# Kernel tuning notes

Hardware: AMD Instinct MI355X
Metric: run time of the kernel (lower is better)

## Reference

```python
import jax, jax.numpy as jnp
import numpy as np

B, V, VD = 4, 256, 3
H_DIM, N_HEADS = 512, 8
HEAD_DIM = H_DIM // N_HEADS
LN_EPS = 1e-5


def _ln(x, g, b):
    m = jnp.mean(x, axis=-1, keepdims=True)
    v = jnp.var(x, axis=-1, keepdims=True)
    return (x - m) * jax.lax.rsqrt(v + LN_EPS) * g + b


def setup_inputs() -> dict:
    key = jax.random.key(0)
    ks = jax.random.split(key, 20)
    s = lambda fan_in: 1.0 / np.sqrt(fan_in)
    return {
        "vertices": jax.random.normal(ks[0], (B, V, VD), jnp.float32),
        # vertex_proj: Linear(3 -> 512)
        "wp": jax.random.uniform(ks[1], (H_DIM, VD), jnp.float32, -s(VD), s(VD)),
        "bp": jax.random.uniform(ks[2], (H_DIM,), jnp.float32, -s(VD), s(VD)),
        # MultiheadAttention packed in-proj (3E, E) and out-proj (E, E)
        "in_w": jax.random.uniform(ks[3], (3 * H_DIM, H_DIM), jnp.float32, -s(H_DIM), s(H_DIM)),
        "in_b": jnp.zeros((3 * H_DIM,), jnp.float32),
        "out_w": jax.random.uniform(ks[4], (H_DIM, H_DIM), jnp.float32, -s(H_DIM), s(H_DIM)),
        "out_b": jnp.zeros((H_DIM,), jnp.float32),
        # edge_mlp: Linear(1024->512), LN(512), GELU, Linear(512->256), LN(256), GELU, Linear(256->1)
        "w1": jax.random.uniform(ks[5], (H_DIM, 2 * H_DIM), jnp.float32, -s(2 * H_DIM), s(2 * H_DIM)),
        "b1": jax.random.uniform(ks[6], (H_DIM,), jnp.float32, -s(2 * H_DIM), s(2 * H_DIM)),
        "g1": jnp.ones((H_DIM,), jnp.float32),
        "be1": jnp.zeros((H_DIM,), jnp.float32),
        "w2": jax.random.uniform(ks[7], (H_DIM // 2, H_DIM), jnp.float32, -s(H_DIM), s(H_DIM)),
        "b2": jax.random.uniform(ks[8], (H_DIM // 2,), jnp.float32, -s(H_DIM), s(H_DIM)),
        "g2": jnp.ones((H_DIM // 2,), jnp.float32),
        "be2": jnp.zeros((H_DIM // 2,), jnp.float32),
        "w3": jax.random.uniform(ks[9], (1, H_DIM // 2), jnp.float32, -s(H_DIM // 2), s(H_DIM // 2)),
        "b3": jax.random.uniform(ks[10], (1,), jnp.float32, -s(H_DIM // 2), s(H_DIM // 2)),
    }


def reference(vertices, wp, bp, in_w, in_b, out_w, out_b,
              w1, b1, g1, be1, w2, b2, g2, be2, w3, b3):
    # vertex projection: [B, V, H]
    x = jnp.einsum("bvd,hd->bvh", vertices, wp) + bp

    # self-attention (eval mode: dropout off)
    qkv = jnp.einsum("bvh,eh->bve", x, in_w) + in_b  # [B, V, 3H]
    q, k, v = jnp.split(qkv, 3, axis=-1)
    q = q.reshape(B, V, N_HEADS, HEAD_DIM)
    k = k.reshape(B, V, N_HEADS, HEAD_DIM)
    v = v.reshape(B, V, N_HEADS, HEAD_DIM)
    scores = jnp.einsum("bqnd,bknd->bnqk", q, k) / np.sqrt(HEAD_DIM)
    attn = jax.nn.softmax(scores, axis=-1)
    ctx = jnp.einsum("bnqk,bknd->bqnd", attn, v).reshape(B, V, H_DIM)
    attended = jnp.einsum("bvh,oh->bvo", ctx, out_w) + out_b
    x = x + attended  # residual

    # gather all upper-triangular vertex pairs: E = V*(V-1)/2
    ii, jj = jnp.triu_indices(V, k=1)
    v1 = x[:, ii, :]  # [B, E, H]
    v2 = x[:, jj, :]
    e = jnp.concatenate([v1, v2], axis=-1)  # [B, E, 2H]

    # edge MLP (exact-erf GELU like torch default)
    h = jnp.einsum("beh,oh->beo", e, w1) + b1
    h = jax.nn.gelu(_ln(h, g1, be1), approximate=False)
    h = jnp.einsum("beh,oh->beo", h, w2) + b2
    h = jax.nn.gelu(_ln(h, g2, be2), approximate=False)
    logits = jnp.einsum("beh,oh->beo", h, w3) + b3  # [B, E, 1]
    return jax.nn.sigmoid(logits[..., 0])  # [B, E]
```

## Files before the change

### kernel.cpp

```cpp
#include <hip/hip_runtime.h>
#include <hip/hip_bf16.h>
#include <hip/hip_fp16.h>

#define B_  4
#define V_  256
#define H_  512
#define E_  32640

typedef _Float16 half8 __attribute__((ext_vector_type(8)));
typedef float    f32x4 __attribute__((ext_vector_type(4)));
typedef unsigned int uint4v __attribute__((ext_vector_type(4)));

__device__ __forceinline__ float gelu_f(float x) {
    float u = x * 0.70710678118654752f;
    float a = fabsf(u);
    float t = __builtin_amdgcn_rcpf(fmaf(0.3275911f, a, 1.0f));
    float poly = t * fmaf(t, fmaf(t, fmaf(t, fmaf(t, 1.061405429f, -1.453152027f),
                                          1.421413741f), -0.284496736f), 0.254829592f);
    float ex = __expf(-u * u);
    float erfa = fmaf(-poly, ex, 1.0f);
    float erfu = copysignf(erfa, u);
    return 0.5f * x * (1.0f + erfu);
}

__device__ __forceinline__ float wred_add(float v) {
    #pragma unroll
    for (int off = 32; off > 0; off >>= 1) v += __shfl_xor(v, off, 64);
    return v;
}

__device__ __forceinline__ void split16(float v, _Float16* hi, _Float16* lo) {
    _Float16 h = (_Float16)v;
    *hi = h; *lo = (_Float16)(v - (float)h);
}

__device__ __forceinline__ unsigned packf(float v) {
    _Float16 h = (_Float16)v;
    _Float16 l = (_Float16)(v - (float)h);
    unsigned hu = (unsigned)__builtin_bit_cast(unsigned short, h);
    unsigned lu = (unsigned)__builtin_bit_cast(unsigned short, l);
    return hu | (lu << 16);
}

__device__ __forceinline__ void unpk8(const unsigned* p, half8& hi, half8& lo) {
    uint4v a = *(const uint4v*)p;
    uint4v b = *(const uint4v*)(p + 4);
    uint4v hw, lw;
    hw[0] = (a[0] & 0xFFFFu) | (a[1] << 16);  lw[0] = (a[0] >> 16) | (a[1] & 0xFFFF0000u);
    hw[1] = (a[2] & 0xFFFFu) | (a[3] << 16);  lw[1] = (a[2] >> 16) | (a[3] & 0xFFFF0000u);
    hw[2] = (b[0] & 0xFFFFu) | (b[1] << 16);  lw[2] = (b[0] >> 16) | (b[1] & 0xFFFF0000u);
    hw[3] = (b[2] & 0xFFFFu) | (b[3] << 16);  lw[3] = (b[2] >> 16) | (b[3] & 0xFFFF0000u);
    hi = __builtin_bit_cast(half8, hw);
    lo = __builtin_bit_cast(half8, lw);
}

__device__ __forceinline__ size_t fmoff(int R, int row, int k) {
    return ((size_t)(k >> 3) * R + row) * 8 + (k & 7);
}

__global__ void k_setup(const float* __restrict__ verts, const float* __restrict__ wp,
                        const float* __restrict__ bp, float* __restrict__ x,
                        _Float16* __restrict__ xfh, _Float16* __restrict__ xfl,
                        const float* __restrict__ w2, _Float16* __restrict__ w2f,
                        int2* __restrict__ etab,
                        const float* __restrict__ in_w, _Float16* __restrict__ iwfh, _Float16* __restrict__ iwfl,
                        const float* __restrict__ out_w, _Float16* __restrict__ owfh, _Float16* __restrict__ owfl,
                        const float* __restrict__ w1, _Float16* __restrict__ w1fh, _Float16* __restrict__ w1fl) {
    int t = blockIdx.x * 256 + threadIdx.x;
    if (t < 524288) {
        int row = t >> 9, k = t & 511;
        const float* vr = verts + row * 3;
        const float* wr = wp + k * 3;
        float val = vr[0] * wr[0] + vr[1] * wr[1] + vr[2] * wr[2] + bp[k];
        x[t] = val;
        size_t fo = fmoff(1024, row, k);
        split16(val, xfh + fo, xfl + fo);
        return;
    }
    t -= 524288;
    if (t < 131072) {
        int col = t >> 9, k = t & 511;
        w2f[fmoff(256, col, k)] = (_Float16)w2[t];
        return;
    }
    t -= 131072;
    if (t < 32640) {
        double disc = (double)(2 * V_ - 1) * (2 * V_ - 1) - 8.0 * (double)t;
        int i = (int)((2 * V_ - 1 - sqrt(disc)) * 0.5);
        if (i < 0) i = 0;
        if (i > V_ - 2) i = V_ - 2;
        while (i < V_ - 2 && (i + 1) * (2 * V_ - 1 - (i + 1)) / 2 <= t) ++i;
        while (i > 0 && i * (2 * V_ - 1 - i) / 2 > t) --i;
        int j = t - i * (2 * V_ - 1 - i) / 2 + i + 1;
        etab[t] = make_int2(i, j);
        return;
    }
    t -= 32640;
    if (t < 786432) {
        int col = t >> 9, k = t & 511;
        size_t fo = fmoff(1536, col, k);
        split16(in_w[t], iwfh + fo, iwfl + fo);
        return;
    }
    t -= 786432;
    if (t < 262144) {
        int col = t >> 9, k = t & 511;
        size_t fo = fmoff(512, col, k);
        split16(out_w[t], owfh + fo, owfl + fo);
        return;
    }
    t -= 262144;
    if (t < 524288) {
        int col = t >> 9, k = t & 511;
        float v = (col < 512) ? w1[col * 1024 + k] : w1[(col - 512) * 1024 + 512 + k];
        size_t fo = fmoff(1024, col, k);
        split16(v, w1fh + fo, w1fl + fo);
    }
}

template<int MODE>
__global__ __launch_bounds__(256) void k_gemm_sp(
        const _Float16* __restrict__ Ahf, const _Float16* __restrict__ Alf,
        const _Float16* __restrict__ Whf, const _Float16* __restrict__ Wlf,
        const float* __restrict__ bias, const float* __restrict__ res,
        float* __restrict__ C, _Float16* __restrict__ Fh, _Float16* __restrict__ Fl,
        float* __restrict__ C2, _Float16* __restrict__ F2h, int N)
{
    const int tid = threadIdx.x;
    const int w = tid >> 6, l = tid & 63;
    const int lr = l & 15, lg = l >> 4;
    const int mg = w >> 1, ng = w & 1;
    const int row0 = blockIdx.y * 64 + mg * 32;
    const int col0 = blockIdx.x * 64 + ng * 32;

    f32x4 acc[2][2] = {};
    for (int kk = 0; kk < 16; ++kk) {
        const int kg = kk * 4 + lg;
        half8 ah[2], al[2], bh[2], bl[2];
        #pragma unroll
        for (int mi = 0; mi < 2; ++mi) {
            size_t off = ((size_t)kg * 1024 + row0 + mi * 16 + lr) * 8;
            if (MODE == 1) {
                unpk8((const unsigned*)Ahf + off, ah[mi], al[mi]);
            } else {
                ah[mi] = *(const half8*)(Ahf + off);
                al[mi] = *(const half8*)(Alf + off);
            }
        }
        #pragma unroll
        for (int ni = 0; ni < 2; ++ni) {
            size_t off = ((size_t)kg * N + col0 + ni * 16 + lr) * 8;
            bh[ni] = *(const half8*)(Whf + off);
            bl[ni] = *(const half8*)(Wlf + off);
        }
        #pragma unroll
        for (int mi = 0; mi < 2; ++mi)
            #pragma unroll
            for (int ni = 0; ni < 2; ++ni) {
                acc[mi][ni] = __builtin_amdgcn_mfma_f32_16x16x32_f16(ah[mi], bh[ni], acc[mi][ni], 0, 0, 0);
                acc[mi][ni] = __builtin_amdgcn_mfma_f32_16x16x32_f16(ah[mi], bl[ni], acc[mi][ni], 0, 0, 0);
                acc[mi][ni] = __builtin_amdgcn_mfma_f32_16x16x32_f16(al[mi], bh[ni], acc[mi][ni], 0, 0, 0);
            }
    }
    #pragma unroll
    for (int mi = 0; mi < 2; ++mi)
        #pragma unroll
        for (int ni = 0; ni < 2; ++ni)
            #pragma unroll
            for (int r = 0; r < 4; ++r) {
                int row = row0 + mi * 16 + lg * 4 + r;
                int col = col0 + ni * 16 + lr;
                float v = acc[mi][ni][r];
                if (MODE == 1) {
                    size_t idx = (size_t)row * 512 + col;
                    v += bias[col] + res[idx];
                    C[idx] = v;
                    size_t fo = fmoff(1024, row, col);
                    split16(v, Fh + fo, Fl + fo);
                } else if (MODE == 2) {
                    if (col < 512) {
                        size_t idx = (size_t)row * 512 + col;
                        v += bias[col];
                        C[idx] = v;
                        Fh[fmoff(1024, row, col)] = (_Float16)v;
                    } else {
                        int c2 = col - 512;
                        C2[(size_t)row * 512 + c2] = v;
                        F2h[fmoff(1024, row, c2)] = (_Float16)v;
                    }
                } else {
                    v += bias[col];
                    int bb = row >> 8, tok = row & 255;
                    if (col < 1024) {
                        int hp = col >> 6, d = col & 63;
                        size_t off = (((size_t)(bb * 16 + hp) * 8 + (d >> 3)) * 256 + tok) * 8 + (d & 7);
                        ((unsigned*)Fh)[off] = packf(v);
                    } else {
                        int c = col - 1024, hp = c >> 6, d = c & 63;
                        size_t off = (((size_t)(bb * 8 + hp) * 32 + (tok >> 3)) * 64 + d) * 8 + (tok & 7);
                        ((unsigned*)C2)[off] = packf(v);
                    }
                }
            }
}

__global__ __launch_bounds__(256) void k_attn(
        const unsigned* __restrict__ QKp, const unsigned* __restrict__ Vp,
        unsigned* __restrict__ ctxp)
{
    extern __shared__ unsigned char smem[];
    const int tid = threadIdx.x;
    const int w = tid >> 6, l = tid & 63;
    const int lr = l & 15, lg = l >> 4;
    const int bh = blockIdx.x >> 2;
    const int b = bh >> 3, h = bh & 7;
    const int qb = blockIdx.x & 3;
    const int q0 = qb * 64 + w * 16;
    unsigned char* ph_base = smem + w * 16384;
    unsigned char* pl_base = ph_base + 8192;

    const size_t qbase = (size_t)(b * 16 + h) * 8;
    const size_t kbase = (size_t)(b * 16 + 8 + h) * 8;
    const size_t vbase = (size_t)(b * 8 + h) * 32;

    half8 qh[2], ql[2];
    #pragma unroll
    for (int ks = 0; ks < 2; ++ks) {
        size_t off = ((qbase + ks * 4 + lg) * 256 + q0 + lr) * 8;
        unpk8(QKp + off, qh[ks], ql[ks]);
    }

    f32x4 sc[16];
    #pragma unroll
    for (int kt = 0; kt < 16; ++kt) {
        f32x4 a = {};
        #pragma unroll
        for (int ks = 0; ks < 2; ++ks) {
            size_t off = ((kbase + ks * 4 + lg) * 256 + kt * 16 + lr) * 8;
            half8 kh, kl;
            unpk8(QKp + off, kh, kl);
            a = __builtin_amdgcn_mfma_f32_16x16x32_f16(qh[ks], kh, a, 0, 0, 0);
            a = __builtin_amdgcn_mfma_f32_16x16x32_f16(qh[ks], kl, a, 0, 0, 0);
            a = __builtin_amdgcn_mfma_f32_16x16x32_f16(ql[ks], kh, a, 0, 0, 0);
        }
        sc[kt] = a;
    }

    float mr[4] = {-1e30f, -1e30f, -1e30f, -1e30f};
    #pragma unroll
    for (int kt = 0; kt < 16; ++kt)
        #pragma unroll
        for (int r = 0; r < 4; ++r) mr[r] = fmaxf(mr[r], sc[kt][r]);
    #pragma unroll
    for (int off = 1; off < 16; off <<= 1)
        #pragma unroll
        for (int r = 0; r < 4; ++r) mr[r] = fmaxf(mr[r], __shfl_xor(mr[r], off, 64));

    float Ls[4] = {};
    #pragma unroll
    for (int kt = 0; kt < 16; ++kt)
        #pragma unroll
        for (int r = 0; r < 4; ++r) {
            float p = __expf((sc[kt][r] - mr[r]) * 0.125f);
            Ls[r] += p;
            _Float16 hp = (_Float16)p;
            _Float16 lp = (_Float16)(p - (float)hp);
            const int row = lg * 4 + r;
            unsigned off = row * 512 + (((unsigned)(kt * 16 + lr) * 2) ^ ((row & 7) << 4));
            *(_Float16*)(ph_base + off) = hp;
            *(_Float16*)(pl_base + off) = lp;
        }
    #pragma unroll
    for (int off = 1; off < 16; off <<= 1)
        #pragma unroll
        for (int r = 0; r < 4; ++r) Ls[r] += __shfl_xor(Ls[r], off, 64);

    __syncthreads();

    f32x4 o[4] = {};
    #pragma unroll
    for (int ks = 0; ks < 8; ++ks) {
        unsigned roff = lr * 512 + (((unsigned)(ks * 64 + lg * 16)) ^ ((lr & 7) << 4));
        half8 pah = *(const half8*)(ph_base + roff);
        half8 pal = *(const half8*)(pl_base + roff);
        #pragma unroll
        for (int nt = 0; nt < 4; ++nt) {
            size_t off = ((vbase + ks * 4 + lg) * 64 + nt * 16 + lr) * 8;
            half8 vbh, vbl;
            unpk8(Vp + off, vbh, vbl);
            o[nt] = __builtin_amdgcn_mfma_f32_16x16x32_f16(pah, vbh, o[nt], 0, 0, 0);
            o[nt] = __builtin_amdgcn_mfma_f32_16x16x32_f16(pah, vbl, o[nt], 0, 0, 0);
            o[nt] = __builtin_amdgcn_mfma_f32_16x16x32_f16(pal, vbh, o[nt], 0, 0, 0);
        }
    }

    float Linv[4];
    #pragma unroll
    for (int r = 0; r < 4; ++r) Linv[r] = 1.0f / Ls[r];
    #pragma unroll
    for (int nt = 0; nt < 4; ++nt)
        #pragma unroll
        for (int r = 0; r < 4; ++r) {
            float val = o[nt][r] * Linv[r];
            int row = b * 256 + q0 + lg * 4 + r;
            int col = h * 64 + nt * 16 + lr;
            ctxp[fmoff(1024, row, col)] = packf(val);
        }
}

__global__ __launch_bounds__(256) void k_pair_stats(
        const _Float16* __restrict__ Ahf, const _Float16* __restrict__ Bhf,
        const float* __restrict__ Amat, const float* __restrict__ Bmat,
        float* __restrict__ P, float2* __restrict__ statsA, float2* __restrict__ statsB) {
    const int bid = blockIdx.x;
    const int tid = threadIdx.x;
    if (bid < 256) {
        const int t = bid * 4 + (tid >> 6);
        const int b = t >> 8, tt = t & 255;
        const int i0 = (tt >> 4) * 16, j0 = (tt & 15) * 16;
        const int l = tid & 63, lr = l & 15, lg = l >> 4;
        f32x4 acc = {};
        for (int kk = 0; kk < 16; ++kk) {
            const int kg = kk * 4 + lg;
            half8 af = *(const half8*)(Ahf + ((size_t)kg * 1024 + b * 256 + i0 + lr) * 8);
            half8 bf = *(const half8*)(Bhf + ((size_t)kg * 1024 + b * 256 + j0 + lr) * 8);
            acc = __builtin_amdgcn_mfma_f32_16x16x32_f16(af, bf, acc, 0, 0, 0);
        }
        #pragma unroll
        for (int r = 0; r < 4; ++r)
            P[((size_t)b << 16) + (size_t)(i0 + lg * 4 + r) * 256 + j0 + lr] = acc[r];
    } else {
        const int sid = bid - 256;
        const int slice = tid >> 4, lane = tid & 15;
        const int m = sid * 16 + slice;
        const float* src = (m < 1024 ? Amat + (size_t)m * 512 : Bmat + (size_t)(m - 1024) * 512);
        float s = 0.0f, sq = 0.0f;
        #pragma unroll
        for (int i = 0; i < 8; ++i) {
            f32x4 v = *(const f32x4*)(src + i * 64 + lane * 4);
            s  += v[0] + v[1] + v[2] + v[3];
            sq += v[0]*v[0] + v[1]*v[1] + v[2]*v[2] + v[3]*v[3];
        }
        #pragma unroll
        for (int off = 8; off > 0; off >>= 1) {
            s  += __shfl_xor(s, off, 64);
            sq += __shfl_xor(sq, off, 64);
        }
        if (lane == 0) {
            if (m < 1024) statsA[m] = make_float2(s, sq);
            else          statsB[m - 1024] = make_float2(s, sq);
        }
    }
}

__global__ __launch_bounds__(512, 8) void k_edge(
        const float* __restrict__ Am, const float* __restrict__ Bm,
        const _Float16* __restrict__ w2f,
        const float* __restrict__ g1, const float* __restrict__ be1,
        const float* __restrict__ b2, const float* __restrict__ g2,
        const float* __restrict__ be2, const float* __restrict__ w3,
        const float* __restrict__ b3, const int2* __restrict__ etab,
        const float2* __restrict__ statsA, const float2* __restrict__ statsB,
        const float* __restrict__ P, float* __restrict__ out)
{
    extern __shared__ unsigned char smem[];
    const int tid = threadIdx.x;
    const int w = tid >> 6;
    const int l = tid & 63;
    const int bid0 = blockIdx.x;
    const int swz = (bid0 & 7) * 510 + (bid0 >> 3);
    const int b  = swz / 1020;
    const int eb = swz % 1020;

    {
        const int e  = w * 4 + (l >> 4);
        const int kq = l & 15;
        int2 ij = etab[eb * 32 + e];
        float2 sa = statsA[b * 256 + ij.x];
        float2 sb = statsB[b * 256 + ij.y];
        float pij = P[((size_t)b << 16) + ((size_t)ij.x << 8) + ij.y];
        float mean = (sa.x + sb.x) * (1.0f / 512.0f);
        float ex2  = (sa.y + sb.y + 2.0f * pij) * (1.0f / 512.0f);
        float rstd = rsqrtf(ex2 - mean * mean + 1e-5f);
        const float* ar = Am + (((size_t)(b * 256 + ij.x)) << 9);
        const float* br = Bm + (((size_t)(b * 256 + ij.y)) << 9);
        #pragma unroll
        for (int t = 0; t < 4; ++t) {
            const int kg = kq + 16 * t;
            const int k0 = kg * 8;
            f32x4 a0 = *(const f32x4*)(ar + k0);
            f32x4 a1 = *(const f32x4*)(ar + k0 + 4);
            f32x4 c0 = *(const f32x4*)(br + k0);
            f32x4 c1 = *(const f32x4*)(br + k0 + 4);
            f32x4 ga = *(const f32x4*)(g1 + k0);
            f32x4 gb = *(const f32x4*)(g1 + k0 + 4);
            f32x4 ea = *(const f32x4*)(be1 + k0);
            f32x4 ebv= *(const f32x4*)(be1 + k0 + 4);
            half8 hv;
            #pragma unroll
            for (int c = 0; c < 4; ++c) {
                float xa = ((a0[c] + c0[c]) - mean) * rstd * ga[c] + ea[c];
                float xb = ((a1[c] + c1[c]) - mean) * rstd * gb[c] + ebv[c];
                hv[c]     = (_Float16)gelu_f(xa);
                hv[c + 4] = (_Float16)gelu_f(xb);
            }
            *(half8*)(smem + kg * 512 + ((e ^ (kg & 7)) << 4)) = hv;
        }
    }
    __syncthreads();

    f32x4 acc[2][2] = {};
    const int lg = l >> 4, lr = l & 15;
    const int col0 = w * 32;
    #pragma unroll
    for (int kk = 0; kk < 16; ++kk) {
        const int kg = kk * 4 + lg;
        half8 bf[2];
        #pragma unroll
        for (int ni = 0; ni < 2; ++ni)
            bf[ni] = *(const half8*)(w2f + ((size_t)kg * 256 + col0 + ni * 16 + lr) * 8);
        half8 af[2];
        #pragma unroll
        for (int mi = 0; mi < 2; ++mi)
            af[mi] = *(const half8*)(smem + kg * 512 + (((mi * 16 + lr) ^ (kg & 7)) << 4));
        #pragma unroll
        for (int mi = 0; mi < 2; ++mi)
            #pragma unroll
            for (int ni = 0; ni < 2; ++ni)
                acc[mi][ni] = __builtin_amdgcn_mfma_f32_16x16x32_f16(af[mi], bf[ni], acc[mi][ni], 0, 0, 0);
    }
    __syncthreads();

    #pragma unroll
    for (int ni = 0; ni < 2; ++ni) {
        const int col = col0 + ni * 16 + lr;
        const float bb = b2[col];
        #pragma unroll
        for (int mi = 0; mi < 2; ++mi)
            #pragma unroll
            for (int r = 0; r < 4; ++r) {
                const int e = mi * 16 + lg * 4 + r;
                *(float*)(smem + e * 1024 + col * 4) = acc[mi][ni][r] + bb;
            }
    }
    __syncthreads();

    {
        const int o0 = l * 4;
        f32x4 g2v = *(const f32x4*)(g2 + o0);
        f32x4 e2v = *(const f32x4*)(be2 + o0);
        f32x4 w3v = *(const f32x4*)(w3 + o0);
        float b3s = b3[0];
        #pragma unroll
        for (int el = 0; el < 4; ++el) {
            const int e = w * 4 + el;
            f32x4 h = *(const f32x4*)(smem + e * 1024 + o0 * 4);
            float s  = h[0] + h[1] + h[2] + h[3];
            float sq = h[0]*h[0] + h[1]*h[1] + h[2]*h[2] + h[3]*h[3];
            s = wred_add(s); sq = wred_add(sq);
            float mean = s * (1.0f / 256.0f);
            float rstd = rsqrtf(sq * (1.0f / 256.0f) - mean * mean + 1e-5f);
            float part = 0.0f;
            #pragma unroll
            for (int c = 0; c < 4; ++c) {
                float xx = (h[c] - mean) * rstd * g2v[c] + e2v[c];
                part += gelu_f(xx) * w3v[c];
            }
            part = wred_add(part);
            if (l == 0)
                out[(size_t)b * E_ + eb * 32 + e] = 1.0f / (1.0f + __expf(-(part + b3s)));
        }
    }
}

extern "C" void kernel_launch(void* const* d_in, const int* in_sizes, int n_in,
                              void* d_out, int out_size, void* d_ws, size_t ws_size,
                              hipStream_t stream) {
    const float* verts = (const float*)d_in[0];
    const float* wp    = (const float*)d_in[1];
    const float* bp    = (const float*)d_in[2];
    const float* in_w  = (const float*)d_in[3];
    const float* in_b  = (const float*)d_in[4];
    const float* out_w = (const float*)d_in[5];
    const float* out_b = (const float*)d_in[6];
    const float* w1    = (const float*)d_in[7];
    const float* b1    = (const float*)d_in[8];
    const float* g1    = (const float*)d_in[9];
    const float* be1   = (const float*)d_in[10];
    const float* w2    = (const float*)d_in[11];
    const float* b2    = (const float*)d_in[12];
    const float* g2    = (const float*)d_in[13];
    const float* be2   = (const float*)d_in[14];
    const float* w3    = (const float*)d_in[15];
    const float* b3    = (const float*)d_in[16];
    float* out = (float*)d_out;

    const size_t MB = 1 << 20;
    char* W = (char*)d_ws;
    float*    x     = (float*)(W + 0);
    _Float16* xfh   = (_Float16*)(W + 2*MB);
    _Float16* xfl   = (_Float16*)(W + 3*MB);
    unsigned* QKp   = (unsigned*)(W + 4*MB);
    unsigned* Vp    = (unsigned*)(W + 8*MB);
    float*    Amat  = (float*)(W + 4*MB);
    float*    Bmat  = (float*)(W + 6*MB);
    _Float16* Ahf   = (_Float16*)(W + 8*MB);
    _Float16* Bhf   = (_Float16*)(W + 9*MB);
    unsigned* ctxp  = (unsigned*)(W + 10*MB);
    _Float16* w2f   = (_Float16*)(W + 12*MB);
    int2*     etab  = (int2*)(W + 12*MB + 256*1024);
    float2*   statsA= (float2*)(W + 12*MB + 512*1024);
    float2*   statsB= (float2*)(W + 12*MB + 520*1024);
    _Float16* iwfh  = (_Float16*)(W + 13*MB);
    _Float16* iwfl  = (_Float16*)(W + 13*MB + 1536*1024);
    _Float16* owfh  = (_Float16*)(W + 16*MB);
    _Float16* owfl  = (_Float16*)(W + 16*MB + 512*1024);
    _Float16* w1fh  = (_Float16*)(W + 17*MB);
    _Float16* w1fl  = (_Float16*)(W + 18*MB);
    float*    P     = (float*)(W + 19*MB);

    k_setup<<<dim3(8832), dim3(256), 0, stream>>>(verts, wp, bp, x, xfh, xfl,
                                                  w2, w2f, etab, in_w, iwfh, iwfl,
                                                  out_w, owfh, owfl, w1, w1fh, w1fl);
    k_gemm_sp<3><<<dim3(24, 16), dim3(256), 0, stream>>>(xfh, xfl, iwfh, iwfl, in_b, nullptr,
                                                         nullptr, (_Float16*)QKp, nullptr,
                                                         (float*)Vp, nullptr, 1536);
    k_attn<<<dim3(128), dim3(256), 65536, stream>>>(QKp, Vp, ctxp);
    k_gemm_sp<1><<<dim3(8, 16), dim3(256), 0, stream>>>((const _Float16*)ctxp, nullptr,
                                                        owfh, owfl, out_b, x,
                                                        x, xfh, xfl, nullptr, nullptr, 512);
    k_gemm_sp<2><<<dim3(16, 16), dim3(256), 0, stream>>>(xfh, xfl, w1fh, w1fl, b1, nullptr,
                                                         Amat, Ahf, nullptr, Bmat, Bhf, 1024);
    k_pair_stats<<<dim3(384), dim3(256), 0, stream>>>(Ahf, Bhf, Amat, Bmat, P, statsA, statsB);
    k_edge<<<dim3(B_ * 1020), dim3(512), 32768, stream>>>(Amat, Bmat, w2f,
                                                          g1, be1, b2, g2, be2, w3, b3,
                                                          etab, statsA, statsB, P, out);
}
```

Baseline: 278.6 us.

## Fuse front-end stages into one cooperative persistent kernel with grid syncs

```diff
diff --git a/kernel.cpp b/kernel.cpp
--- a/kernel.cpp
+++ b/kernel.cpp
@@ -1,6 +1,9 @@
 #include <hip/hip_runtime.h>
+#include <hip/hip_cooperative_groups.h>
 #include <hip/hip_bf16.h>
 #include <hip/hip_fp16.h>
+
+namespace cg = cooperative_groups;
 
 #define B_  4
 #define V_  256
@@ -58,29 +61,34 @@
     return ((size_t)(k >> 3) * R + row) * 8 + (k & 7);
 }
 
-__global__ void k_setup(const float* __restrict__ verts, const float* __restrict__ wp,
-                        const float* __restrict__ bp, float* __restrict__ x,
-                        _Float16* __restrict__ xfh, _Float16* __restrict__ xfl,
-                        const float* __restrict__ w2, _Float16* __restrict__ w2f,
-                        int2* __restrict__ etab,
-                        const float* __restrict__ in_w, _Float16* __restrict__ iwfh, _Float16* __restrict__ iwfl,
-                        const float* __restrict__ out_w, _Float16* __restrict__ owfh, _Float16* __restrict__ owfl,
-                        const float* __restrict__ w1, _Float16* __restrict__ w1fh, _Float16* __restrict__ w1fl) {
-    int t = blockIdx.x * 256 + threadIdx.x;
+struct FrontParams {
+    const float *verts, *wp, *bp;
+    float *x; _Float16 *xfh, *xfl;
+    const float *w2; _Float16 *w2f; int2 *etab;
+    const float *in_w; _Float16 *iwfh, *iwfl;
+    const float *out_w; _Float16 *owfh, *owfl;
+    const float *w1; _Float16 *w1fh, *w1fl;
+    const float *in_b, *out_b, *b1;
+    unsigned *QKp, *Vp, *ctxp;
+    float *Amat, *Bmat; _Float16 *Ahf, *Bhf;
+    float *P; float2 *statsA, *statsB;
+};
+
+__device__ __forceinline__ void setup_item(int t, const FrontParams& p) {
     if (t < 524288) {
         int row = t >> 9, k = t & 511;
-        const float* vr = verts + row * 3;
-        const float* wr = wp + k * 3;
-        float val = vr[0] * wr[0] + vr[1] * wr[1] + vr[2] * wr[2] + bp[k];
-        x[t] = val;
+        const float* vr = p.verts + row * 3;
+        const float* wr = p.wp + k * 3;
+        float val = vr[0] * wr[0] + vr[1] * wr[1] + vr[2] * wr[2] + p.bp[k];
+        p.x[t] = val;
         size_t fo = fmoff(1024, row, k);
-        split16(val, xfh + fo, xfl + fo);
+        split16(val, p.xfh + fo, p.xfl + fo);
         return;
     }
     t -= 524288;
     if (t < 131072) {
         int col = t >> 9, k = t & 511;
-        w2f[fmoff(256, col, k)] = (_Float16)w2[t];
+        p.w2f[fmoff(256, col, k)] = (_Float16)p.w2[(size_t)col * 512 + k];
         return;
     }
     t -= 131072;
@@ -92,133 +100,118 @@
         while (i < V_ - 2 && (i + 1) * (2 * V_ - 1 - (i + 1)) / 2 <= t) ++i;
         while (i > 0 && i * (2 * V_ - 1 - i) / 2 > t) --i;
         int j = t - i * (2 * V_ - 1 - i) / 2 + i + 1;
-        etab[t] = make_int2(i, j);
+        p.etab[t] = make_int2(i, j);
         return;
     }
     t -= 32640;
     if (t < 786432) {
         int col = t >> 9, k = t & 511;
         size_t fo = fmoff(1536, col, k);
-        split16(in_w[t], iwfh + fo, iwfl + fo);
+        split16(p.in_w[t], p.iwfh + fo, p.iwfl + fo);
         return;
     }
     t -= 786432;
     if (t < 262144) {
         int col = t >> 9, k = t & 511;
         size_t fo = fmoff(512, col, k);
-        split16(out_w[t], owfh + fo, owfl + fo);
+        split16(p.out_w[t], p.owfh + fo, p.owfl + fo);
         return;
     }
     t -= 262144;
-    if (t < 524288) {
+    {
         int col = t >> 9, k = t & 511;
-        float v = (col < 512) ? w1[col * 1024 + k] : w1[(col - 512) * 1024 + 512 + k];
+        float v = (col < 512) ? p.w1[col * 1024 + k] : p.w1[(col - 512) * 1024 + 512 + k];
         size_t fo = fmoff(1024, col, k);
-        split16(v, w1fh + fo, w1fl + fo);
+        split16(v, p.w1fh + fo, p.w1fl + fo);
     }
 }
 
 template<int MODE>
-__global__ __launch_bounds__(256) void k_gemm_sp(
-        const _Float16* __restrict__ Ahf, const _Float16* __restrict__ Alf,
-        const _Float16* __restrict__ Whf, const _Float16* __restrict__ Wlf,
-        const float* __restrict__ bias, const float* __restrict__ res,
-        float* __restrict__ C, _Float16* __restrict__ Fh, _Float16* __restrict__ Fl,
-        float* __restrict__ C2, _Float16* __restrict__ F2h, int N)
+__device__ __forceinline__ void gemm_tile(
+        int tile, int tilesN, int N,
+        const _Float16* Ahf, const _Float16* Alf,
+        const _Float16* Whf, const _Float16* Wlf,
+        const float* bias, const float* res,
+        float* C, _Float16* Fh, _Float16* Fl, float* C2, _Float16* F2h,
+        int w, int l)
 {
-    const int tid = threadIdx.x;
-    const int w = tid >> 6, l = tid & 63;
     const int lr = l & 15, lg = l >> 4;
     const int mg = w >> 1, ng = w & 1;
-    const int row0 = blockIdx.y * 64 + mg * 32;
-    const int col0 = blockIdx.x * 64 + ng * 32;
-
-    f32x4 acc[2][2] = {};
+    const int row0 = (tile / tilesN) * 32 + mg * 16;
+    const int col0 = (tile % tilesN) * 64 + ng * 32;
+
+    f32x4 acc[2] = {};
     for (int kk = 0; kk < 16; ++kk) {
         const int kg = kk * 4 + lg;
-        half8 ah[2], al[2], bh[2], bl[2];
-        #pragma unroll
-        for (int mi = 0; mi < 2; ++mi) {
-            size_t off = ((size_t)kg * 1024 + row0 + mi * 16 + lr) * 8;
+        half8 ah, al, bh[2], bl[2];
+        size_t aoff = ((size_t)kg * 1024 + row0 + lr) * 8;
+        if (MODE == 1) {
+            unpk8((const unsigned*)Ahf + aoff, ah, al);
+        } else {
+            ah = *(const half8*)(Ahf + aoff);
+            al = *(const half8*)(Alf + aoff);
+        }
+        #pragma unroll
+        for (int ni = 0; ni < 2; ++ni) {
+            size_t boff = ((size_t)kg * N + col0 + ni * 16 + lr) * 8;
+            bh[ni] = *(const half8*)(Whf + boff);
+            bl[ni] = *(const half8*)(Wlf + boff);
+        }
+        #pragma unroll
+        for (int ni = 0; ni < 2; ++ni) {
+            acc[ni] = __builtin_amdgcn_mfma_f32_16x16x32_f16(ah, bh[ni], acc[ni], 0, 0, 0);
+            acc[ni] = __builtin_amdgcn_mfma_f32_16x16x32_f16(ah, bl[ni], acc[ni], 0, 0, 0);
+            acc[ni] = __builtin_amdgcn_mfma_f32_16x16x32_f16(al, bh[ni], acc[ni], 0, 0, 0);
+        }
+    }
+    #pragma unroll
+    for (int ni = 0; ni < 2; ++ni)
+        #pragma unroll
+        for (int r = 0; r < 4; ++r) {
+            int row = row0 + lg * 4 + r;
+            int col = col0 + ni * 16 + lr;
+            float v = acc[ni][r];
             if (MODE == 1) {
-                unpk8((const unsigned*)Ahf + off, ah[mi], al[mi]);
+                size_t idx = (size_t)row * 512 + col;
+                v += bias[col] + res[idx];
+                C[idx] = v;
+                size_t fo = fmoff(1024, row, col);
+                split16(v, Fh + fo, Fl + fo);
+            } else if (MODE == 2) {
+                if (col < 512) {
+                    size_t idx = (size_t)row * 512 + col;
+                    v += bias[col];
+                    C[idx] = v;
+                    Fh[fmoff(1024, row, col)] = (_Float16)v;
+                } else {
+                    int c2 = col - 512;
+                    C2[(size_t)row * 512 + c2] = v;
+                    F2h[fmoff(1024, row, c2)] = (_Float16)v;
+                }
             } else {
-                ah[mi] = *(const half8*)(Ahf + off);
-                al[mi] = *(const half8*)(Alf + off);
-            }
-        }
-        #pragma unroll
-        for (int ni = 0; ni < 2; ++ni) {
-            size_t off = ((size_t)kg * N + col0 + ni * 16 + lr) * 8;
-            bh[ni] = *(const half8*)(Whf + off);
-            bl[ni] = *(const half8*)(Wlf + off);
-        }
-        #pragma unroll
-        for (int mi = 0; mi < 2; ++mi)
-            #pragma unroll
-            for (int ni = 0; ni < 2; ++ni) {
-                acc[mi][ni] = __builtin_amdgcn_mfma_f32_16x16x32_f16(ah[mi], bh[ni], acc[mi][ni], 0, 0, 0);
-                acc[mi][ni] = __builtin_amdgcn_mfma_f32_16x16x32_f16(ah[mi], bl[ni], acc[mi][ni], 0, 0, 0);
-                acc[mi][ni] = __builtin_amdgcn_mfma_f32_16x16x32_f16(al[mi], bh[ni], acc[mi][ni], 0, 0, 0);
-            }
-    }
-    #pragma unroll
-    for (int mi = 0; mi < 2; ++mi)
-        #pragma unroll
-        for (int ni = 0; ni < 2; ++ni)
-            #pragma unroll
-            for (int r = 0; r < 4; ++r) {
-                int row = row0 + mi * 16 + lg * 4 + r;
-                int col = col0 + ni * 16 + lr;
-                float v = acc[mi][ni][r];
-                if (MODE == 1) {
-                    size_t idx = (size_t)row * 512 + col;
-                    v += bias[col] + res[idx];
-                    C[idx] = v;
-                    size_t fo = fmoff(1024, row, col);
-                    split16(v, Fh + fo, Fl + fo);
-                } else if (MODE == 2) {
-                    if (col < 512) {
-                        size_t idx = (size_t)row * 512 + col;
-                        v += bias[col];
-                        C[idx] = v;
-                        Fh[fmoff(1024, row, col)] = (_Float16)v;
-                    } else {
-                        int c2 = col - 512;
-                        C2[(size_t)row * 512 + c2] = v;
-                        F2h[fmoff(1024, row, c2)] = (_Float16)v;
-                    }
+                v += bias[col];
+                int bb = row >> 8, tok = row & 255;
+                if (col < 1024) {
+                    int hp = col >> 6, d = col & 63;
+                    size_t off = (((size_t)(bb * 16 + hp) * 8 + (d >> 3)) * 256 + tok) * 8 + (d & 7);
+                    ((unsigned*)Fh)[off] = packf(v);
                 } else {
-                    v += bias[col];
-                    int bb = row >> 8, tok = row & 255;
-                    if (col < 1024) {
-                        int hp = col >> 6, d = col & 63;
-                        size_t off = (((size_t)(bb * 16 + hp) * 8 + (d >> 3)) * 256 + tok) * 8 + (d & 7);
-                        ((unsigned*)Fh)[off] = packf(v);
-                    } else {
-                        int c = col - 1024, hp = c >> 6, d = c & 63;
-                        size_t off = (((size_t)(bb * 8 + hp) * 32 + (tok >> 3)) * 64 + d) * 8 + (tok & 7);
-                        ((unsigned*)C2)[off] = packf(v);
-                    }
+                    int c = col - 1024, hp = c >> 6, d = c & 63;
+                    size_t off = (((size_t)(bb * 8 + hp) * 32 + (tok >> 3)) * 64 + d) * 8 + (tok & 7);
+                    ((unsigned*)C2)[off] = packf(v);
                 }
             }
-}
-
-__global__ __launch_bounds__(256) void k_attn(
-        const unsigned* __restrict__ QKp, const unsigned* __restrict__ Vp,
-        unsigned* __restrict__ ctxp)
-{
-    extern __shared__ unsigned char smem[];
-    const int tid = threadIdx.x;
-    const int w = tid >> 6, l = tid & 63;
+        }
+}
+
+__device__ __forceinline__ void attn_job(int job, int w, int l,
+                                         unsigned (&pb)[16][132],
+                                         const FrontParams& p) {
     const int lr = l & 15, lg = l >> 4;
-    const int bh = blockIdx.x >> 2;
+    const int bh = job >> 2;
     const int b = bh >> 3, h = bh & 7;
-    const int qb = blockIdx.x & 3;
+    const int qb = job & 3;
     const int q0 = qb * 64 + w * 16;
-    unsigned char* ph_base = smem + w * 16384;
-    unsigned char* pl_base = ph_base + 8192;
-
     const size_t qbase = (size_t)(b * 16 + h) * 8;
     const size_t kbase = (size_t)(b * 16 + 8 + h) * 8;
     const size_t vbase = (size_t)(b * 8 + h) * 32;
@@ -227,10 +220,9 @@
     #pragma unroll
     for (int ks = 0; ks < 2; ++ks) {
         size_t off = ((qbase + ks * 4 + lg) * 256 + q0 + lr) * 8;
-        unpk8(QKp + off, qh[ks], ql[ks]);
-    }
-
-    f32x4 sc[16];
+        unpk8(p.QKp + off, qh[ks], ql[ks]);
+    }
+    float mr[4] = {-1e30f, -1e30f, -1e30f, -1e30f};
     #pragma unroll
     for (int kt = 0; kt < 16; ++kt) {
         f32x4 a = {};
@@ -238,62 +230,62 @@
         for (int ks = 0; ks < 2; ++ks) {
             size_t off = ((kbase + ks * 4 + lg) * 256 + kt * 16 + lr) * 8;
             half8 kh, kl;
-            unpk8(QKp + off, kh, kl);
+            unpk8(p.QKp + off, kh, kl);
             a = __builtin_amdgcn_mfma_f32_16x16x32_f16(qh[ks], kh, a, 0, 0, 0);
             a = __builtin_amdgcn_mfma_f32_16x16x32_f16(qh[ks], kl, a, 0, 0, 0);
             a = __builtin_amdgcn_mfma_f32_16x16x32_f16(ql[ks], kh, a, 0, 0, 0);
         }
-        sc[kt] = a;
-    }
-
-    float mr[4] = {-1e30f, -1e30f, -1e30f, -1e30f};
-    #pragma unroll
-    for (int kt = 0; kt < 16; ++kt)
-        #pragma unroll
-        for (int r = 0; r < 4; ++r) mr[r] = fmaxf(mr[r], sc[kt][r]);
+        #pragma unroll
+        for (int r = 0; r < 4; ++r) mr[r] = fmaxf(mr[r], a[r]);
+    }
     #pragma unroll
     for (int off = 1; off < 16; off <<= 1)
         #pragma unroll
         for (int r = 0; r < 4; ++r) mr[r] = fmaxf(mr[r], __shfl_xor(mr[r], off, 64));
 
     float Ls[4] = {};
-    #pragma unroll
-    for (int kt = 0; kt < 16; ++kt)
-        #pragma unroll
-        for (int r = 0; r < 4; ++r) {
-            float p = __expf((sc[kt][r] - mr[r]) * 0.125f);
-            Ls[r] += p;
-            _Float16 hp = (_Float16)p;
-            _Float16 lp = (_Float16)(p - (float)hp);
-            const int row = lg * 4 + r;
-            unsigned off = row * 512 + (((unsigned)(kt * 16 + lr) * 2) ^ ((row & 7) << 4));
-            *(_Float16*)(ph_base + off) = hp;
-            *(_Float16*)(pl_base + off) = lp;
-        }
+    f32x4 o[4] = {};
+    #pragma unroll
+    for (int H = 0; H < 2; ++H) {
+        #pragma unroll
+        for (int kt2 = 0; kt2 < 8; ++kt2) {
+            const int kt = H * 8 + kt2;
+            f32x4 a = {};
+            #pragma unroll
+            for (int ks = 0; ks < 2; ++ks) {
+                size_t off = ((kbase + ks * 4 + lg) * 256 + kt * 16 + lr) * 8;
+                half8 kh, kl;
+                unpk8(p.QKp + off, kh, kl);
+                a = __builtin_amdgcn_mfma_f32_16x16x32_f16(qh[ks], kh, a, 0, 0, 0);
+                a = __builtin_amdgcn_mfma_f32_16x16x32_f16(qh[ks], kl, a, 0, 0, 0);
+                a = __builtin_amdgcn_mfma_f32_16x16x32_f16(ql[ks], kh, a, 0, 0, 0);
+            }
+            #pragma unroll
+            for (int r = 0; r < 4; ++r) {
+                float pv = __expf((a[r] - mr[r]) * 0.125f);
+                Ls[r] += pv;
+                pb[lg * 4 + r][kt2 * 16 + lr] = packf(pv);
+            }
+        }
+        #pragma unroll
+        for (int ks = 0; ks < 4; ++ks) {
+            half8 pah, pal;
+            unpk8(&pb[lr][ks * 32 + lg * 8], pah, pal);
+            #pragma unroll
+            for (int nt = 0; nt < 4; ++nt) {
+                size_t off = ((vbase + (size_t)(H * 4 + ks) * 4 + lg) * 64 + nt * 16 + lr) * 8;
+                half8 vbh, vbl;
+                unpk8(p.Vp + off, vbh, vbl);
+                o[nt] = __builtin_amdgcn_mfma_f32_16x16x32_f16(pah, vbh, o[nt], 0, 0, 0);
+                o[nt] = __builtin_amdgcn_mfma_f32_16x16x32_f16(pah, vbl, o[nt], 0, 0, 0);
+                o[nt] = __builtin_amdgcn_mfma_f32_16x16x32_f16(pal, vbh, o[nt], 0, 0, 0);
+            }
+        }
+    }
     #pragma unroll
     for (int off = 1; off < 16; off <<= 1)
         #pragma unroll
         for (int r = 0; r < 4; ++r) Ls[r] += __shfl_xor(Ls[r], off, 64);
-
-    __syncthreads();
-
-    f32x4 o[4] = {};
-    #pragma unroll
-    for (int ks = 0; ks < 8; ++ks) {
-        unsigned roff = lr * 512 + (((unsigned)(ks * 64 + lg * 16)) ^ ((lr & 7) << 4));
-        half8 pah = *(const half8*)(ph_base + roff);
-        half8 pal = *(const half8*)(pl_base + roff);
-        #pragma unroll
-        for (int nt = 0; nt < 4; ++nt) {
-            size_t off = ((vbase + ks * 4 + lg) * 64 + nt * 16 + lr) * 8;
-            half8 vbh, vbl;
-            unpk8(Vp + off, vbh, vbl);
-            o[nt] = __builtin_amdgcn_mfma_f32_16x16x32_f16(pah, vbh, o[nt], 0, 0, 0);
-            o[nt] = __builtin_amdgcn_mfma_f32_16x16x32_f16(pah, vbl, o[nt], 0, 0, 0);
-            o[nt] = __builtin_amdgcn_mfma_f32_16x16x32_f16(pal, vbh, o[nt], 0, 0, 0);
-        }
-    }
-
     float Linv[4];
     #pragma unroll
     for (int r = 0; r < 4; ++r) Linv[r] = 1.0f / Ls[r];
@@ -304,36 +296,32 @@
             float val = o[nt][r] * Linv[r];
             int row = b * 256 + q0 + lg * 4 + r;
             int col = h * 64 + nt * 16 + lr;
-            ctxp[fmoff(1024, row, col)] = packf(val);
-        }
-}
-
-__global__ __launch_bounds__(256) void k_pair_stats(
-        const _Float16* __restrict__ Ahf, const _Float16* __restrict__ Bhf,
-        const float* __restrict__ Amat, const float* __restrict__ Bmat,
-        float* __restrict__ P, float2* __restrict__ statsA, float2* __restrict__ statsB) {
-    const int bid = blockIdx.x;
-    const int tid = threadIdx.x;
-    if (bid < 256) {
-        const int t = bid * 4 + (tid >> 6);
+            p.ctxp[fmoff(1024, row, col)] = packf(val);
+        }
+}
+
+__device__ __forceinline__ void pair_job(int job, int tid, const FrontParams& p) {
+    const int w = tid >> 6, l = tid & 63;
+    const int lr = l & 15, lg = l >> 4;
+    if (job < 256) {
+        const int t = job * 4 + w;
         const int b = t >> 8, tt = t & 255;
         const int i0 = (tt >> 4) * 16, j0 = (tt & 15) * 16;
-        const int l = tid & 63, lr = l & 15, lg = l >> 4;
         f32x4 acc = {};
         for (int kk = 0; kk < 16; ++kk) {
             const int kg = kk * 4 + lg;
-            half8 af = *(const half8*)(Ahf + ((size_t)kg * 1024 + b * 256 + i0 + lr) * 8);
-            half8 bf = *(const half8*)(Bhf + ((size_t)kg * 1024 + b * 256 + j0 + lr) * 8);
+            half8 af = *(const half8*)(p.Ahf + ((size_t)kg * 1024 + b * 256 + i0 + lr) * 8);
+            half8 bf = *(const half8*)(p.Bhf + ((size_t)kg * 1024 + b * 256 + j0 + lr) * 8);
             acc = __builtin_amdgcn_mfma_f32_16x16x32_f16(af, bf, acc, 0, 0, 0);
         }
         #pragma unroll
         for (int r = 0; r < 4; ++r)
-            P[((size_t)b << 16) + (size_t)(i0 + lg * 4 + r) * 256 + j0 + lr] = acc[r];
+            p.P[((size_t)b << 16) + (size_t)(i0 + lg * 4 + r) * 256 + j0 + lr] = acc[r];
     } else {
-        const int sid = bid - 256;
+        const int sid = job - 256;
         const int slice = tid >> 4, lane = tid & 15;
         const int m = sid * 16 + slice;
-        const float* src = (m < 1024 ? Amat + (size_t)m * 512 : Bmat + (size_t)(m - 1024) * 512);
+        const float* src = (m < 1024 ? p.Amat + (size_t)m * 512 : p.Bmat + (size_t)(m - 1024) * 512);
         float s = 0.0f, sq = 0.0f;
         #pragma unroll
         for (int i = 0; i < 8; ++i) {
@@ -347,10 +335,72 @@
             sq += __shfl_xor(sq, off, 64);
         }
         if (lane == 0) {
-            if (m < 1024) statsA[m] = make_float2(s, sq);
-            else          statsB[m - 1024] = make_float2(s, sq);
-        }
-    }
+            if (m < 1024) p.statsA[m] = make_float2(s, sq);
+            else          p.statsB[m - 1024] = make_float2(s, sq);
+        }
+    }
+}
+
+__global__ __launch_bounds__(256, 4) void k_front(FrontParams p) {
+    __shared__ unsigned pbuf[4][16][132];
+    cg::grid_group grid = cg::this_grid();
+    const int tid = threadIdx.x;
+    const int w = tid >> 6, l = tid & 63;
+    const int nb = gridDim.x;
+
+    for (int t0 = blockIdx.x * 256 + tid; t0 < 2260864; t0 += nb * 256)
+        setup_item(t0, p);
+    grid.sync();
+
+    for (int tile = blockIdx.x; tile < 768; tile += nb)
+        gemm_tile<3>(tile, 24, 1536, p.xfh, p.xfl, p.iwfh, p.iwfl, p.in_b, nullptr,
+                     nullptr, (_Float16*)p.QKp, nullptr, (float*)p.Vp, nullptr, w, l);
+    grid.sync();
+
+    for (int job = blockIdx.x; job < 128; job += nb)
+        attn_job(job, w, l, pbuf[w], p);
+    grid.sync();
+
+    for (int tile = blockIdx.x; tile < 256; tile += nb)
+        gemm_tile<1>(tile, 8, 512, (const _Float16*)p.ctxp, nullptr, p.owfh, p.owfl,
+                     p.out_b, p.x, p.x, p.xfh, p.xfl, nullptr, nullptr, w, l);
+    grid.sync();
+
+    for (int tile = blockIdx.x; tile < 512; tile += nb)
+        gemm_tile<2>(tile, 16, 1024, p.xfh, p.xfl, p.w1fh, p.w1fl, p.b1, nullptr,
+                     p.Amat, p.Ahf, nullptr, p.Bmat, p.Bhf, w, l);
+    grid.sync();
+
+    for (int job = blockIdx.x; job < 384; job += nb)
+        pair_job(job, tid, p);
+}
+
+__global__ __launch_bounds__(256) void k_s0(FrontParams p) {
+    int t = blockIdx.x * 256 + threadIdx.x;
+    if (t < 2260864) setup_item(t, p);
+}
+__global__ __launch_bounds__(256) void k_s2(FrontParams p) {
+    const int tid = threadIdx.x;
+    gemm_tile<3>(blockIdx.x, 24, 1536, p.xfh, p.xfl, p.iwfh, p.iwfl, p.in_b, nullptr,
+                 nullptr, (_Float16*)p.QKp, nullptr, (float*)p.Vp, nullptr, tid >> 6, tid & 63);
+}
+__global__ __launch_bounds__(256) void k_s4(FrontParams p) {
+    __shared__ unsigned pbuf[4][16][132];
+    const int tid = threadIdx.x;
+    attn_job(blockIdx.x, tid >> 6, tid & 63, pbuf[tid >> 6], p);
+}
+__global__ __launch_bounds__(256) void k_s6(FrontParams p) {
+    const int tid = threadIdx.x;
+    gemm_tile<1>(blockIdx.x, 8, 512, (const _Float16*)p.ctxp, nullptr, p.owfh, p.owfl,
+                 p.out_b, p.x, p.x, p.xfh, p.xfl, nullptr, nullptr, tid >> 6, tid & 63);
+}
+__global__ __launch_bounds__(256) void k_s8(FrontParams p) {
+    const int tid = threadIdx.x;
+    gemm_tile<2>(blockIdx.x, 16, 1024, p.xfh, p.xfl, p.w1fh, p.w1fl, p.b1, nullptr,
+                 p.Amat, p.Ahf, nullptr, p.Bmat, p.Bhf, tid >> 6, tid & 63);
+}
+__global__ __launch_bounds__(256) void k_s10(FrontParams p) {
+    pair_job(blockIdx.x, threadIdx.x, p);
 }
 
 __global__ __launch_bounds__(512, 8) void k_edge(
@@ -497,42 +547,48 @@
 
     const size_t MB = 1 << 20;
     char* W = (char*)d_ws;
-    float*    x     = (float*)(W + 0);
-    _Float16* xfh   = (_Float16*)(W + 2*MB);
-    _Float16* xfl   = (_Float16*)(W + 3*MB);
-    unsigned* QKp   = (unsigned*)(W + 4*MB);
-    unsigned* Vp    = (unsigned*)(W + 8*MB);
-    float*    Amat  = (float*)(W + 4*MB);
-    float*    Bmat  = (float*)(W + 6*MB);
-    _Float16* Ahf   = (_Float16*)(W + 8*MB);
-    _Float16* Bhf   = (_Float16*)(W + 9*MB);
-    unsigned* ctxp  = (unsigned*)(W + 10*MB);
-    _Float16* w2f   = (_Float16*)(W + 12*MB);
-    int2*     etab  = (int2*)(W + 12*MB + 256*1024);
-    float2*   statsA= (float2*)(W + 12*MB + 512*1024);
-    float2*   statsB= (float2*)(W + 12*MB + 520*1024);
-    _Float16* iwfh  = (_Float16*)(W + 13*MB);
-    _Float16* iwfl  = (_Float16*)(W + 13*MB + 1536*1024);
-    _Float16* owfh  = (_Float16*)(W + 16*MB);
-    _Float16* owfl  = (_Float16*)(W + 16*MB + 512*1024);
-    _Float16* w1fh  = (_Float16*)(W + 17*MB);
-    _Float16* w1fl  = (_Float16*)(W + 18*MB);
-    float*    P     = (float*)(W + 19*MB);
-
-    k_setup<<<dim3(8832), dim3(256), 0, stream>>>(verts, wp, bp, x, xfh, xfl,
-                                                  w2, w2f, etab, in_w, iwfh, iwfl,
-                                                  out_w, owfh, owfl, w1, w1fh, w1fl);
-    k_gemm_sp<3><<<dim3(24, 16), dim3(256), 0, stream>>>(xfh, xfl, iwfh, iwfl, in_b, nullptr,
-                                                         nullptr, (_Float16*)QKp, nullptr,
-                                                         (float*)Vp, nullptr, 1536);
-    k_attn<<<dim3(128), dim3(256), 65536, stream>>>(QKp, Vp, ctxp);
-    k_gemm_sp<1><<<dim3(8, 16), dim3(256), 0, stream>>>((const _Float16*)ctxp, nullptr,
-                                                        owfh, owfl, out_b, x,
-                                                        x, xfh, xfl, nullptr, nullptr, 512);
-    k_gemm_sp<2><<<dim3(16, 16), dim3(256), 0, stream>>>(xfh, xfl, w1fh, w1fl, b1, nullptr,
-                                                         Amat, Ahf, nullptr, Bmat, Bhf, 1024);
-    k_pair_stats<<<dim3(384), dim3(256), 0, stream>>>(Ahf, Bhf, Amat, Bmat, P, statsA, statsB);
-    k_edge<<<dim3(B_ * 1020), dim3(512), 32768, stream>>>(Amat, Bmat, w2f,
+    FrontParams fp;
+    fp.verts = verts; fp.wp = wp; fp.bp = bp;
+    fp.x     = (float*)(W + 0);
+    fp.xfh   = (_Float16*)(W + 2*MB);
+    fp.xfl   = (_Float16*)(W + 3*MB);
+    fp.QKp   = (unsigned*)(W + 4*MB);
+    fp.Vp    = (unsigned*)(W + 8*MB);
+    fp.Amat  = (float*)(W + 4*MB);
+    fp.Bmat  = (float*)(W + 6*MB);
+    fp.Ahf   = (_Float16*)(W + 8*MB);
+    fp.Bhf   = (_Float16*)(W + 9*MB);
+    fp.ctxp  = (unsigned*)(W + 10*MB);
+    fp.w2    = w2;
+    fp.w2f   = (_Float16*)(W + 12*MB);
+    fp.etab  = (int2*)(W + 12*MB + 256*1024);
+    fp.statsA= (float2*)(W + 12*MB + 512*1024);
+    fp.statsB= (float2*)(W + 12*MB + 520*1024);
+    fp.in_w  = in_w;
+    fp.iwfh  = (_Float16*)(W + 13*MB);
+    fp.iwfl  = (_Float16*)(W + 13*MB + 1536*1024);
+    fp.out_w = out_w;
+    fp.owfh  = (_Float16*)(W + 16*MB);
+    fp.owfl  = (_Float16*)(W + 16*MB + 512*1024);
+    fp.w1    = w1;
+    fp.w1fh  = (_Float16*)(W + 17*MB);
+    fp.w1fl  = (_Float16*)(W + 18*MB);
+    fp.P     = (float*)(W + 19*MB);
+    fp.in_b  = in_b; fp.out_b = out_b; fp.b1 = b1;
+
+    void* args[] = { &fp };
+    hipError_t err = hipLaunchCooperativeKernel((void*)k_front, dim3(768), dim3(256),
+                                                args, 0, stream);
+    if (err != hipSuccess) {
+        k_s0 <<<dim3(8832), dim3(256), 0, stream>>>(fp);
+        k_s2 <<<dim3(768),  dim3(256), 0, stream>>>(fp);
+        k_s4 <<<dim3(128),  dim3(256), 0, stream>>>(fp);
+        k_s6 <<<dim3(256),  dim3(256), 0, stream>>>(fp);
+        k_s8 <<<dim3(512),  dim3(256), 0, stream>>>(fp);
+        k_s10<<<dim3(384),  dim3(256), 0, stream>>>(fp);
+    }
+
+    k_edge<<<dim3(B_ * 1020), dim3(512), 32768, stream>>>(fp.Amat, fp.Bmat, fp.w2f,
                                                           g1, be1, b2, g2, be2, w3, b3,
-                                                          etab, statsA, statsB, P, out);
-}
+                                                          fp.etab, fp.statsA, fp.statsB, fp.P, out);
+}
```

Measured after the change: 742.3 us. +166.5%, slower.
